# Optimization experiments

Hardware: AMD Instinct MI355X
Metric: run time of the kernel (lower is better)

Reference implementation:

```python
import jax, jax.numpy as jnp
import numpy as np

B, LATENT, H, OUT, T, L = 4096, 128, 256, 88, 64, 5  # batch, latent, hidden, output(88 keys), seq_len, num_layers


def setup_inputs() -> dict:
    key = jax.random.key(0)
    ks = jax.random.split(key, 8)
    sc = 1.0 / np.sqrt(H)
    n = lambda k, shp, s: (jax.random.normal(k, shp, jnp.float32) * s)
    return {
        "x": jax.random.normal(ks[0], (B, LATENT), jnp.float32),
        "linear_w": n(ks[1], (H, LATENT), 1.0 / np.sqrt(LATENT)),
        "linear_b": jnp.zeros((H,), jnp.float32),
        # PyTorch LSTM layout: [4H, in] with gate order i, f, g, o. Layer-0 input size == H.
        "w_ih": n(ks[2], (L, 4 * H, H), sc),
        "w_hh": n(ks[3], (L, 4 * H, H), sc),
        "b_ih": n(ks[4], (L, 4 * H), sc),
        "b_hh": n(ks[5], (L, 4 * H), sc),
        "out_w": n(ks[6], (OUT, H), sc),
        "out_b": jnp.zeros((OUT,), jnp.float32),
    }


def _lstm_cell(gates, c):
    # gates: [B, 4H] pre-activation, PyTorch order i, f, g, o
    i, f, g, o = jnp.split(gates, 4, axis=-1)
    c_new = jax.nn.sigmoid(f) * c + jax.nn.sigmoid(i) * jnp.tanh(g)
    h_new = jax.nn.sigmoid(o) * jnp.tanh(c_new)
    return h_new, c_new


def _lstm(xp, w_ih, w_hh, b_ih, b_hh):
    # xp: [B, H] latent projection, repeated over T timesteps (constant input).
    bsz = xp.shape[0]
    gx0 = xp @ w_ih[0].T + b_ih[0]  # layer-0 input gates, constant across time [B, 4H]
    h0 = jnp.zeros((L, bsz, H), xp.dtype)
    c0 = jnp.zeros((L, bsz, H), xp.dtype)

    def step(carry, _):
        h, c = carry  # [L, B, H]
        hs, cs = [], []
        layer_in_gates = gx0
        for l in range(L):  # fixed small loop over structurally distinct layers
            if l > 0:
                layer_in_gates = hs[-1] @ w_ih[l].T + b_ih[l]
            gates = layer_in_gates + h[l] @ w_hh[l].T + b_hh[l]
            hl, cl = _lstm_cell(gates, c[l])
            hs.append(hl)
            cs.append(cl)
        return (jnp.stack(hs), jnp.stack(cs)), hs[-1]

    _, ys = jax.lax.scan(step, (h0, c0), None, length=T)  # ys: [T, B, H]
    return ys.transpose(1, 0, 2)  # [B, T, H]


def reference(x, linear_w, linear_b, w_ih, w_hh, b_ih, b_hh, out_w, out_b):
    xp = x @ linear_w.T + linear_b  # [B, H]; unsqueeze+repeat folded into constant gx0
    y = _lstm(xp, w_ih, w_hh, b_ih, b_hh)  # [B, T, H]
    return jax.nn.sigmoid(y @ out_w.T + out_b)  # [B, T, OUT]
```

## Files before the change

### kernel.cpp

```cpp
#include <hip/hip_runtime.h>
#include <hip/hip_bf16.h>
#include <cstdint>

#define B_ 4096
#define H_ 256
#define G_ 1024
#define T_ 64
#define L_ 5

typedef __hip_bfloat16 bf16;
typedef __bf16 bf16x8 __attribute__((ext_vector_type(8)));
typedef float f32x4 __attribute__((ext_vector_type(4)));

#define OFF_WCOMB   0ull
#define OFF_WIH0R   5242880ull
#define OFF_LWB     5767168ull
#define OFF_XB      5832704ull
#define OFF_OBW     6881280ull
#define OFF_BIAS    6930432ull
#define OFF_XP      6950912ull
#define OFF_GX0     9048064ull
#define OFF_H0      25825280ull
#define OFF_H1      34213888ull
#define OFF_C1      42602496ull
#define OFF_YS      63574016ull
#define OFF_C0      199888896ull
#define TOTAL_WS    220860416ull
#define SLOT_H      2097152ull
#define SLOT_C      4194304ull

__device__ __forceinline__ bf16* h_ptr(char* ws, int l, int p) {
  return (bf16*)(ws + (p ? OFF_H1 : OFF_H0) + (size_t)l * SLOT_H);
}
__device__ __forceinline__ float* c_ptr(char* ws, int l, int p) {
  return (float*)(ws + (p ? OFF_C1 : OFF_C0) + (size_t)l * SLOT_C);
}
__device__ __forceinline__ bf16* ys_ptr(char* ws, int s) {
  return (bf16*)(ws + OFF_YS + (size_t)s * SLOT_H);
}

__device__ __forceinline__ float frcp(float x) { return __builtin_amdgcn_rcpf(x); }
__device__ __forceinline__ float fsig(float x) { return frcp(1.0f + __expf(-x)); }
__device__ __forceinline__ float ftanh(float x) { return 1.0f - 2.0f * frcp(1.0f + __expf(2.0f * x)); }

__device__ __forceinline__ void gload16(const void* g, void* l) {
  __builtin_amdgcn_global_load_lds((const __attribute__((address_space(1))) void*)g,
                                   (__attribute__((address_space(3))) void*)l, 16, 0, 0);
}

__device__ __forceinline__ void stage_tile(char* dst, const bf16* src, long stride, int koff,
                                           int wv, int lane) {
#pragma unroll
  for (int i = 0; i < 4; ++i) {
    int r = 32 * wv + 8 * i + (lane >> 3);
    int cb = ((lane & 7) << 4) ^ ((r & 7) << 4);
    const bf16* g = src + (long)r * stride + koff + (cb >> 1);
    char* ld = dst + (32 * wv + 8 * i) * 128;
    gload16(g, ld);
  }
}

template <int OUTMODE>
__device__ void gemm_core(const bf16* __restrict__ A1, int lda1,
                          const bf16* __restrict__ A2,
                          const bf16* __restrict__ W, int ldw, int K,
                          const float* __restrict__ bias,
                          const float* __restrict__ acc2d,
                          float* __restrict__ outF, bf16* __restrict__ outB, int ldo,
                          const float* __restrict__ cIn, float* __restrict__ cOut,
                          bf16* __restrict__ hOut,
                          int mtile, int ntile, char* smem) {
  const int tid = threadIdx.x;
  const int lane = tid & 63, wv = tid >> 6;
  const int wrow = wv >> 1, wcol = wv & 1;
  const int row0 = mtile * 128;
  const int n0 = ntile * 128;

  char* As = smem;
  char* Bs = smem + 16384;

  f32x4 acc[4][4];
  if (acc2d) {
#pragma unroll
    for (int m = 0; m < 4; m++)
#pragma unroll
      for (int n = 0; n < 4; n++)
#pragma unroll
        for (int r = 0; r < 4; r++) {
          int row = row0 + wrow * 64 + 16 * m + ((lane >> 4) << 2) + r;
          int col = n0 + wcol * 64 + 16 * n + (lane & 15);
          acc[m][n][r] = acc2d[(long)row * G_ + col];
        }
  } else {
#pragma unroll
    for (int n = 0; n < 4; n++) {
      int col = n0 + wcol * 64 + 16 * n + (lane & 15);
      float bv = bias ? bias[col] : 0.0f;
#pragma unroll
      for (int m = 0; m < 4; m++)
#pragma unroll
        for (int r = 0; r < 4; r++) acc[m][n][r] = bv;
    }
  }

  const int nkb = K >> 6;
  for (int kb = 0; kb < nkb; ++kb) {
    if (kb < 4) stage_tile(As, A1 + (long)row0 * lda1, lda1, kb * 64, wv, lane);
    else        stage_tile(As, A2 + (long)row0 * 256,  256,  kb * 64 - 256, wv, lane);
    stage_tile(Bs, W + (long)n0 * ldw, ldw, kb * 64, wv, lane);
    __syncthreads();
#pragma unroll
    for (int ks = 0; ks < 2; ++ks) {
      bf16x8 af[4], bfr[4];
#pragma unroll
      for (int m = 0; m < 4; m++) {
        int r = wrow * 64 + 16 * m + (lane & 15);
        int cb = (ks * 64 + ((lane >> 4) << 4)) ^ ((r & 7) << 4);
        af[m] = *(const bf16x8*)(As + r * 128 + cb);
      }
#pragma unroll
      for (int n = 0; n < 4; n++) {
        int r = wcol * 64 + 16 * n + (lane & 15);
        int cb = (ks * 64 + ((lane >> 4) << 4)) ^ ((r & 7) << 4);
        bfr[n] = *(const bf16x8*)(Bs + r * 128 + cb);
      }
#pragma unroll
      for (int m = 0; m < 4; m++)
#pragma unroll
        for (int n = 0; n < 4; n++)
          acc[m][n] = __builtin_amdgcn_mfma_f32_16x16x32_bf16(af[m], bfr[n], acc[m][n], 0, 0, 0);
    }
    __syncthreads();
  }

  if (OUTMODE == 0 || OUTMODE == 1) {
#pragma unroll
    for (int m = 0; m < 4; m++)
#pragma unroll
      for (int n = 0; n < 4; n++)
#pragma unroll
        for (int r = 0; r < 4; r++) {
          int row = row0 + wrow * 64 + 16 * m + ((lane >> 4) << 2) + r;
          int col = n0 + wcol * 64 + 16 * n + (lane & 15);
          if (OUTMODE == 0) outF[(long)row * ldo + col] = acc[m][n][r];
          else              outB[(long)row * ldo + col] = __float2bfloat16(acc[m][n][r]);
        }
  } else {
#pragma unroll
    for (int h = 0; h < 2; ++h) {
      if (wcol == h) {
#pragma unroll
        for (int m = 0; m < 4; m++)
#pragma unroll
          for (int n = 0; n < 4; n++)
#pragma unroll
            for (int r = 0; r < 4; r++) {
              int rr = wrow * 64 + 16 * m + ((lane >> 4) << 2) + r;
              int cc2 = 16 * n + (lane & 15);
              *(float*)(smem + rr * 256 + ((cc2 << 2) ^ ((rr & 7) << 4))) = acc[m][n][r];
            }
      }
      __syncthreads();
      int j2 = tid & 15;
      int rb = tid >> 4;
#pragma unroll
      for (int i = 0; i < 8; i++) {
        int rr = rb + 16 * i;
        f32x4 g4 = *(const f32x4*)(smem + rr * 256 + ((j2 << 4) ^ ((rr & 7) << 4)));
        int row = row0 + rr;
        int jj = ntile * 32 + 16 * h + j2;
        float cold = cIn ? cIn[(long)row * H_ + jj] : 0.0f;
        float cn = fsig(g4[1]) * cold + fsig(g4[0]) * ftanh(g4[2]);
        float hn = fsig(g4[3]) * ftanh(cn);
        cOut[(long)row * H_ + jj] = cn;
        hOut[(long)row * H_ + jj] = __float2bfloat16(hn);
      }
      if (h == 0) __syncthreads();
    }
  }
}

template <int OUTMODE>
__global__ __launch_bounds__(256) void gemm_generic(const bf16* A1, int lda1,
                                                    const bf16* W, int ldw, int K,
                                                    const float* bias,
                                                    float* outF, bf16* outB, int ldo) {
  __shared__ __align__(16) char smem[32768];
  int mtile = blockIdx.x & 31;
  int ntile = blockIdx.x >> 5;
  gemm_core<OUTMODE>(A1, lda1, A1 , W, ldw, K, bias, nullptr,
                     outF, outB, ldo, nullptr, nullptr, nullptr, mtile, ntile, smem);
}

__global__ __launch_bounds__(256) void lstm_diag(int d, char* __restrict__ ws) {
  __shared__ __align__(16) char smem[32768];
  int l0 = d > 63 ? d - 63 : 0;
  int l = l0 + blockIdx.y;
  int t = d - l;
  int bid = blockIdx.x;
  int wg = (bid & 7) * 32 + (bid >> 3);
  int w = wg & 31, q = wg >> 5;
  int mtile = q * 4 + (w & 3);
  int ntile = w >> 2;
  int sp = (t & 1) ^ 1, op = t & 1;
  bool tz = (t == 0);

  const bf16* wc = (const bf16*)(ws + OFF_WCOMB) + (long)l * G_ * 512;
  const bf16* A1; const bf16* A2; int K;
  const float* bias = nullptr; const float* acc2d = nullptr;
  if (l == 0) {
    A1 = h_ptr(ws, 0, sp); A2 = A1;
    K = tz ? 0 : 256;
    acc2d = (const float*)(ws + OFF_GX0);
  } else {
    A1 = h_ptr(ws, l - 1, op);
    A2 = (l == 4) ? ys_ptr(ws, t) : h_ptr(ws, l, sp);
    K = tz ? 256 : 512;
    bias = (const float*)(ws + OFF_BIAS) + l * G_;
  }
  const float* cIn = tz ? nullptr : c_ptr(ws, l, sp);
  float* cOut = c_ptr(ws, l, op);
  bf16* hOut = (l == 4) ? ys_ptr(ws, t + 1) : h_ptr(ws, l, op);

  gemm_core<2>(A1, 256, A2, wc, 512, K, bias, acc2d,
               nullptr, nullptr, 0, cIn, cOut, hOut, mtile, ntile, smem);
}

__global__ __launch_bounds__(256) void proj_kernel(char* __restrict__ ws,
                                                   const float* __restrict__ ob,
                                                   float* __restrict__ out) {
  __shared__ __align__(16) char smem[49152];
  int mtile = blockIdx.x;
  int t = blockIdx.y;
  const bf16* ys = ys_ptr(ws, t + 1);
  const char* obw = (const char*)(ws + OFF_OBW);
  int tid = threadIdx.x, lane = tid & 63, wv = tid >> 6;
#pragma unroll
  for (int i = 0; i < 12; i++) {
    int r = wv * 24 + i * 2 + (lane >> 5);
    int cb = ((lane & 31) << 4) ^ ((r & 7) << 4);
    gload16(obw + r * 512 + cb, smem + (wv * 24 + i * 2) * 512);
  }
  __syncthreads();
  f32x4 acc[2][6];
#pragma unroll
  for (int m = 0; m < 2; m++)
#pragma unroll
    for (int n = 0; n < 6; n++)
#pragma unroll
      for (int r = 0; r < 4; r++) acc[m][n][r] = 0.0f;
  const char* arow = (const char*)(ys + (long)(mtile * 128) * 256);
  for (int kk = 0; kk < 256; kk += 32) {
    bf16x8 af[2], bfr[6];
#pragma unroll
    for (int m = 0; m < 2; m++) {
      int r = wv * 32 + 16 * m + (lane & 15);
      af[m] = *(const bf16x8*)(arow + (long)r * 512 + kk * 2 + ((lane >> 4) << 4));
    }
#pragma unroll
    for (int n = 0; n < 6; n++) {
      int r = 16 * n + (lane & 15);
      int cb = (kk * 2 + ((lane >> 4) << 4)) ^ ((r & 7) << 4);
      bfr[n] = *(const bf16x8*)(smem + r * 512 + cb);
    }
#pragma unroll
    for (int m = 0; m < 2; m++)
#pragma unroll
      for (int n = 0; n < 6; n++)
        acc[m][n] = __builtin_amdgcn_mfma_f32_16x16x32_bf16(af[m], bfr[n], acc[m][n], 0, 0, 0);
  }
#pragma unroll
  for (int m = 0; m < 2; m++)
#pragma unroll
    for (int n = 0; n < 6; n++)
#pragma unroll
      for (int r = 0; r < 4; r++) {
        int row = mtile * 128 + wv * 32 + 16 * m + ((lane >> 4) << 2) + r;
        int o = 16 * n + (lane & 15);
        if (o < 88) {
          float v = acc[m][n][r] + ob[o];
          out[((long)row * T_ + t) * 88 + o] = fsig(v);
        }
      }
}

__global__ void prep_kernel(const float* __restrict__ x, const float* __restrict__ lw,
                            const float* __restrict__ wih, const float* __restrict__ whh,
                            const float* __restrict__ bih, const float* __restrict__ bhh,
                            const float* __restrict__ ow, char* __restrict__ ws) {
  bf16* xb = (bf16*)(ws + OFF_XB);
  bf16* lwb = (bf16*)(ws + OFF_LWB);
  bf16* wcomb = (bf16*)(ws + OFF_WCOMB);
  bf16* wih0r = (bf16*)(ws + OFF_WIH0R);
  bf16* obw = (bf16*)(ws + OFF_OBW);
  float* bias = (float*)(ws + OFF_BIAS);
  const int S0 = 524288, S1 = 32768, S2 = 2621440, S3 = 262144, S4 = 24576, S5 = 5120;
  const int total = S0 + S1 + S2 + S3 + S4 + S5;
  for (int i = blockIdx.x * blockDim.x + threadIdx.x; i < total; i += gridDim.x * blockDim.x) {
    int idx = i;
    if (idx < S0) { xb[idx] = __float2bfloat16(x[idx]); continue; }
    idx -= S0;
    if (idx < S1) { lwb[idx] = __float2bfloat16(lw[idx]); continue; }
    idx -= S1;
    if (idx < S2) {
      int l = idx >> 19;
      int rem = idx & 524287;
      int n = rem >> 9;
      int k = rem & 511;
      int row = (n & 3) * 256 + (n >> 2);
      float v;
      if (l == 0) v = (k < 256) ? whh[row * 256 + k] : 0.0f;
      else        v = (k < 256) ? wih[(l * 1024 + row) * 256 + k]
                                : whh[(l * 1024 + row) * 256 + (k - 256)];
      wcomb[idx] = __float2bfloat16(v); continue;
    }
    idx -= S2;
    if (idx < S3) {
      int n = idx >> 8, k = idx & 255;
      int row = (n & 3) * 256 + (n >> 2);
      wih0r[idx] = __float2bfloat16(wih[row * 256 + k]); continue;
    }
    idx -= S3;
    if (idx < S4) {
      int r = idx >> 8, k = idx & 255;
      obw[idx] = __float2bfloat16(r < 88 ? ow[r * 256 + k] : 0.0f); continue;
    }
    idx -= S4;
    {
      int l = idx >> 10, n = idx & 1023;
      int row = (n & 3) * 256 + (n >> 2);
      bias[idx] = bih[l * 1024 + row] + bhh[l * 1024 + row];
    }
  }
}

extern "C" void kernel_launch(void* const* d_in, const int* in_sizes, int n_in,
                              void* d_out, int out_size, void* d_ws, size_t ws_size,
                              hipStream_t stream) {
  const float* x   = (const float*)d_in[0];
  const float* lw  = (const float*)d_in[1];
  const float* lb  = (const float*)d_in[2];
  const float* wih = (const float*)d_in[3];
  const float* whh = (const float*)d_in[4];
  const float* bih = (const float*)d_in[5];
  const float* bhh = (const float*)d_in[6];
  const float* ow  = (const float*)d_in[7];
  const float* ob  = (const float*)d_in[8];
  char* ws = (char*)d_ws;
  float* out = (float*)d_out;

  if (ws_size < TOTAL_WS) return;

  prep_kernel<<<2048, 256, 0, stream>>>(x, lw, wih, whh, bih, bhh, ow, ws);

  gemm_generic<1><<<dim3(64), 256, 0, stream>>>(
      (const bf16*)(ws + OFF_XB), 128, (const bf16*)(ws + OFF_LWB), 128, 128,
      lb, nullptr, (bf16*)(ws + OFF_XP), 256);

  gemm_generic<0><<<dim3(256), 256, 0, stream>>>(
      (const bf16*)(ws + OFF_XP), 256, (const bf16*)(ws + OFF_WIH0R), 256, 256,
      (const float*)(ws + OFF_BIAS), (float*)(ws + OFF_GX0), nullptr, 1024);

  for (int d = 0; d < 68; ++d) {
    int lo = d > 63 ? d - 63 : 0;
    int hi = d < 4 ? d : 4;
    int nc = hi - lo + 1;
    lstm_diag<<<dim3(256, nc), 256, 0, stream>>>(d, ws);
  }

  proj_kernel<<<dim3(32, 64), 256, 0, stream>>>(ws, ob, out);
}
```

Baseline: 2.987 ms.

## Double-buffer weight tiles, load activations directly to registers, drop t==0 special case

The GEMM core now double-buffers the weight tile in LDS and prefetches the next k-block while computing the current one. The activation operand is read straight from global memory into registers instead of going through LDS, which removes one barrier per k-block. The t==0 special case is replaced by an up-front memset that zeroes the state buffers, and lstm_diag gets a min-blocks-per-CU launch bound of 3 plus a plain, unswizzled tile mapping. The trade-offs are uncoalesced per-lane global reads for the activations, some extra work at t=0, and possibly worse L2 locality without the swizzle.

```diff
diff --git a/kernel.cpp b/kernel.cpp
--- a/kernel.cpp
+++ b/kernel.cpp
@@ -26,6 +26,7 @@
 #define OFF_YS      63574016ull
 #define OFF_C0      199888896ull
 #define TOTAL_WS    220860416ull
+#define ZERO_BYTES  31457280ull
 #define SLOT_H      2097152ull
 #define SLOT_C      4194304ull
 
@@ -76,8 +77,7 @@
   const int row0 = mtile * 128;
   const int n0 = ntile * 128;
 
-  char* As = smem;
-  char* Bs = smem + 16384;
+  char* Bs[2] = { smem, smem + 16384 };
 
   f32x4 acc[4][4];
   if (acc2d) {
@@ -104,34 +104,43 @@
   }
 
   const int nkb = K >> 6;
+  stage_tile(Bs[0], W + (long)n0 * ldw, ldw, 0, wv, lane);
+
   for (int kb = 0; kb < nkb; ++kb) {
-    if (kb < 4) stage_tile(As, A1 + (long)row0 * lda1, lda1, kb * 64, wv, lane);
-    else        stage_tile(As, A2 + (long)row0 * 256,  256,  kb * 64 - 256, wv, lane);
-    stage_tile(Bs, W + (long)n0 * ldw, ldw, kb * 64, wv, lane);
     __syncthreads();
+    if (kb + 1 < nkb)
+      stage_tile(Bs[(kb + 1) & 1], W + (long)n0 * ldw, ldw, (kb + 1) * 64, wv, lane);
+
+    const bf16* Asrc; long las;
+    if (kb < 4) { Asrc = A1 + kb * 64;        las = lda1; }
+    else        { Asrc = A2 + (kb * 64 - 256); las = 256; }
+    bf16x8 af[2][4];
+#pragma unroll
+    for (int m = 0; m < 4; m++) {
+      const bf16* p = Asrc + (long)(row0 + wrow * 64 + 16 * m + (lane & 15)) * las
+                    + ((lane >> 4) << 3);
+      af[0][m] = *(const bf16x8*)p;
+      af[1][m] = *(const bf16x8*)(p + 32);
+    }
+
+    char* Bb = Bs[kb & 1];
 #pragma unroll
     for (int ks = 0; ks < 2; ++ks) {
-      bf16x8 af[4], bfr[4];
-#pragma unroll
-      for (int m = 0; m < 4; m++) {
-        int r = wrow * 64 + 16 * m + (lane & 15);
-        int cb = (ks * 64 + ((lane >> 4) << 4)) ^ ((r & 7) << 4);
-        af[m] = *(const bf16x8*)(As + r * 128 + cb);
-      }
+      bf16x8 bfr[4];
 #pragma unroll
       for (int n = 0; n < 4; n++) {
         int r = wcol * 64 + 16 * n + (lane & 15);
         int cb = (ks * 64 + ((lane >> 4) << 4)) ^ ((r & 7) << 4);
-        bfr[n] = *(const bf16x8*)(Bs + r * 128 + cb);
+        bfr[n] = *(const bf16x8*)(Bb + r * 128 + cb);
       }
 #pragma unroll
       for (int m = 0; m < 4; m++)
 #pragma unroll
         for (int n = 0; n < 4; n++)
-          acc[m][n] = __builtin_amdgcn_mfma_f32_16x16x32_bf16(af[m], bfr[n], acc[m][n], 0, 0, 0);
-    }
-    __syncthreads();
-  }
+          acc[m][n] = __builtin_amdgcn_mfma_f32_16x16x32_bf16(af[ks][m], bfr[n], acc[m][n], 0, 0, 0);
+    }
+  }
+  __syncthreads();
 
   if (OUTMODE == 0 || OUTMODE == 1) {
 #pragma unroll
@@ -169,7 +178,7 @@
         f32x4 g4 = *(const f32x4*)(smem + rr * 256 + ((j2 << 4) ^ ((rr & 7) << 4)));
         int row = row0 + rr;
         int jj = ntile * 32 + 16 * h + j2;
-        float cold = cIn ? cIn[(long)row * H_ + jj] : 0.0f;
+        float cold = cIn[(long)row * H_ + jj];
         float cn = fsig(g4[1]) * cold + fsig(g4[0]) * ftanh(g4[2]);
         float hn = fsig(g4[3]) * ftanh(cn);
         cOut[(long)row * H_ + jj] = cn;
@@ -192,33 +201,28 @@
                      outF, outB, ldo, nullptr, nullptr, nullptr, mtile, ntile, smem);
 }
 
-__global__ __launch_bounds__(256) void lstm_diag(int d, char* __restrict__ ws) {
+__global__ __launch_bounds__(256, 3) void lstm_diag(int d, char* __restrict__ ws) {
   __shared__ __align__(16) char smem[32768];
   int l0 = d > 63 ? d - 63 : 0;
   int l = l0 + blockIdx.y;
   int t = d - l;
-  int bid = blockIdx.x;
-  int wg = (bid & 7) * 32 + (bid >> 3);
-  int w = wg & 31, q = wg >> 5;
-  int mtile = q * 4 + (w & 3);
-  int ntile = w >> 2;
+  int mtile = blockIdx.x & 31;
+  int ntile = blockIdx.x >> 5;
   int sp = (t & 1) ^ 1, op = t & 1;
-  bool tz = (t == 0);
 
   const bf16* wc = (const bf16*)(ws + OFF_WCOMB) + (long)l * G_ * 512;
-  const bf16* A1; const bf16* A2; int K;
+  const bf16* A1; const bf16* A2 = nullptr; int K;
   const float* bias = nullptr; const float* acc2d = nullptr;
   if (l == 0) {
-    A1 = h_ptr(ws, 0, sp); A2 = A1;
-    K = tz ? 0 : 256;
+    A1 = h_ptr(ws, 0, sp); A2 = A1; K = 256;
     acc2d = (const float*)(ws + OFF_GX0);
   } else {
     A1 = h_ptr(ws, l - 1, op);
     A2 = (l == 4) ? ys_ptr(ws, t) : h_ptr(ws, l, sp);
-    K = tz ? 256 : 512;
+    K = 512;
     bias = (const float*)(ws + OFF_BIAS) + l * G_;
   }
-  const float* cIn = tz ? nullptr : c_ptr(ws, l, sp);
+  const float* cIn = c_ptr(ws, l, sp);
   float* cOut = c_ptr(ws, l, op);
   bf16* hOut = (l == 4) ? ys_ptr(ws, t + 1) : h_ptr(ws, l, op);
 
@@ -351,6 +355,7 @@
 
   if (ws_size < TOTAL_WS) return;
 
+  hipMemsetAsync(ws + OFF_H1, 0, ZERO_BYTES, stream);
   prep_kernel<<<2048, 256, 0, stream>>>(x, lw, wih, whh, bih, bhh, ow, ws);
 
   gemm_generic<1><<<dim3(64), 256, 0, stream>>>(
```

Result: slower. 3.947 ms (+32.1%).
